# Kernel tuning notes

Hardware: AMD Instinct MI355X
Metric: run time of the kernel (lower is better)

Reference implementation:

```python
import jax, jax.numpy as jnp
import numpy as np

B, H, S, D = 2, 16, 1024, 64

def setup_inputs() -> dict:
    key = jax.random.key(0)
    k1, k2 = jax.random.split(key)
    # x1 is the output of a softmax (attention probabilities): non-negative, rows sum to 1
    logits = jax.random.normal(k1, (B, H, S, S), dtype=jnp.float32)
    x1 = jax.nn.softmax(logits, axis=-1)
    x2 = jax.random.normal(k2, (B, H, S, D), dtype=jnp.float32)
    return {"x1": x1, "x2": x2}

def reference(x1, x2):
    # Forward of EfficientMemoryGEMMWithSoftmax: exact batched GEMM.
    # (The outlier/low-bit compression only affects what is cached for backward;
    #  the forward output is the exact product.)
    return jnp.einsum('bhsk,bhkd->bhsd', x1, x2)
```

## Files before the change

### kernel.cpp

```cpp
#include <hip/hip_runtime.h>
#include <hip/hip_bf16.h>

typedef __attribute__((ext_vector_type(8))) short short8_t;
typedef __attribute__((ext_vector_type(4))) short short4_t;
typedef __attribute__((ext_vector_type(4))) float f32x4;

#define S_DIM   1024
#define D_DIM   64
#define BM      64
#define KC      64
#define NCHUNK  (S_DIM / KC)
#define BSTRIDE 72
#define THREADS 512

__device__ __forceinline__ ushort f2bf(float f) {
    __hip_bfloat16 h = __float2bfloat16(f);
    return __builtin_bit_cast(ushort, h);
}

#define SYNC() do { \
    __builtin_amdgcn_sched_barrier(0); \
    asm volatile("s_waitcnt lgkmcnt(0)"); \
    __builtin_amdgcn_s_barrier(); \
    __builtin_amdgcn_sched_barrier(0); \
} while (0)

__global__ __launch_bounds__(THREADS, 4)
void gemm_sm_kernel(const float* __restrict__ x1,
                    const float* __restrict__ x2,
                    float* __restrict__ out) {
    __shared__ ushort lds_a[2][BM * KC];
    __shared__ ushort lds_b[2][D_DIM * BSTRIDE];

    const int tid = threadIdx.x;
    const int bid = blockIdx.x;
    const int xcd = bid & 7;
    const int q   = bid >> 3;
    const int batch   = xcd * 4 + (q & 3);
    const int rowtile = q >> 2;
    const int row0    = rowtile * BM;

    const float* Abase = x1 + (size_t)batch * (S_DIM * S_DIM) + (size_t)row0 * S_DIM;
    const float* Bbase = x2 + (size_t)batch * (S_DIM * D_DIM);
    float*       Cbase = out + (size_t)batch * (S_DIM * D_DIM) + (size_t)row0 * D_DIM;

    const int w = tid >> 6;
    const int l = tid & 63;

    const int ar  = tid >> 3;
    const int ak8 = (tid & 7) * 8;
    const float* aptr = Abase + (size_t)ar * S_DIM + ak8;
    const int aw = (ar * KC + ak8) ^ ((ar & 7) << 3);

    const int bd  = l;
    const int bk0 = w * 4;

    const int wm = w >> 1, wn = w & 1;
    const int fr = l & 15, fg = l >> 4;
    int aidx[2], bidx[2][2];
    {
        const int row = wm * 16 + fr;
        #pragma unroll
        for (int ks = 0; ks < 2; ++ks)
            aidx[ks] = (row * KC + ks * 32 + fg * 8) ^ ((row & 7) << 3);
    }
    #pragma unroll
    for (int nf = 0; nf < 2; ++nf) {
        const int col = wn * 32 + nf * 16 + fr;
        #pragma unroll
        for (int ks = 0; ks < 2; ++ks)
            bidx[nf][ks] = col * BSTRIDE + ks * 32 + fg * 8;
    }

    float a0[8], a1[8], b0[8], b1[8];

    auto load_chunk = [&](int t, float (&A)[8], float (&B)[8]) {
        const float* p = aptr + t * KC;
        #pragma unroll
        for (int i = 0; i < 2; ++i) {
            float4 v = *reinterpret_cast<const float4*>(p + i * 4);
            A[i * 4 + 0] = v.x; A[i * 4 + 1] = v.y;
            A[i * 4 + 2] = v.z; A[i * 4 + 3] = v.w;
        }
        const float* bp = Bbase + (size_t)t * KC * D_DIM + bd;
        #pragma unroll
        for (int i = 0; i < 2; ++i)
            #pragma unroll
            for (int j = 0; j < 4; ++j)
                B[i * 4 + j] = bp[(bk0 + 32 * i + j) * D_DIM];
    };

    auto store_chunk = [&](ushort* la, ushort* lb,
                           const float (&A)[8], const float (&B)[8]) {
        short8_t v0;
        #pragma unroll
        for (int j = 0; j < 8; ++j) v0[j] = (short)f2bf(A[j]);
        *reinterpret_cast<short8_t*>(&la[aw]) = v0;
        #pragma unroll
        for (int i = 0; i < 2; ++i) {
            short4_t bv;
            #pragma unroll
            for (int j = 0; j < 4; ++j) bv[j] = (short)f2bf(B[i * 4 + j]);
            *reinterpret_cast<short4_t*>(&lb[bd * BSTRIDE + bk0 + 32 * i]) = bv;
        }
    };

    f32x4 acc[2];
    acc[0] = f32x4{0.f, 0.f, 0.f, 0.f};
    acc[1] = f32x4{0.f, 0.f, 0.f, 0.f};

    auto compute = [&](const ushort* la, const ushort* lb) {
        short8_t af[2], bf[2][2];
        #pragma unroll
        for (int ks = 0; ks < 2; ++ks)
            af[ks] = *reinterpret_cast<const short8_t*>(&la[aidx[ks]]);
        #pragma unroll
        for (int nf = 0; nf < 2; ++nf)
            #pragma unroll
            for (int ks = 0; ks < 2; ++ks)
                bf[nf][ks] = *reinterpret_cast<const short8_t*>(&lb[bidx[nf][ks]]);
        #pragma unroll
        for (int ks = 0; ks < 2; ++ks)
            #pragma unroll
            for (int nf = 0; nf < 2; ++nf)
                acc[nf] = __builtin_amdgcn_mfma_f32_16x16x32_bf16(
                    af[ks], bf[nf][ks], acc[nf], 0, 0, 0);
    };

    load_chunk(0, a0, b0);
    load_chunk(1, a1, b1);
    store_chunk(&lds_a[0][0], &lds_b[0][0], a0, b0);
    SYNC();

    #pragma unroll 1
    for (int ti = 0; ti < NCHUNK; ti += 2) {
        if (ti + 2 < NCHUNK) load_chunk(ti + 2, a0, b0);
        store_chunk(&lds_a[1][0], &lds_b[1][0], a1, b1);
        compute(&lds_a[0][0], &lds_b[0][0]);
        SYNC();

        if (ti + 3 < NCHUNK) load_chunk(ti + 3, a1, b1);
        if (ti + 2 < NCHUNK) store_chunk(&lds_a[0][0], &lds_b[0][0], a0, b0);
        compute(&lds_a[1][0], &lds_b[1][0]);
        SYNC();
    }

    #pragma unroll
    for (int nf = 0; nf < 2; ++nf)
        #pragma unroll
        for (int j = 0; j < 4; ++j) {
            const int r = wm * 16 + fg * 4 + j;
            const int c = wn * 32 + nf * 16 + fr;
            Cbase[(size_t)r * D_DIM + c] = acc[nf][j];
        }
}

extern "C" void kernel_launch(void* const* d_in, const int* in_sizes, int n_in,
                              void* d_out, int out_size, void* d_ws, size_t ws_size,
                              hipStream_t stream) {
    const float* x1 = (const float*)d_in[0];
    const float* x2 = (const float*)d_in[1];
    float* out = (float*)d_out;
    dim3 grid(512), block(THREADS);
    gemm_sm_kernel<<<grid, block, 0, stream>>>(x1, x2, out);
}
```

Baseline: 28.32 us.

## Load A fragments directly from global into registers, dropping the A LDS staging

```diff
diff --git a/kernel.cpp b/kernel.cpp
--- a/kernel.cpp
+++ b/kernel.cpp
@@ -29,7 +29,6 @@
 void gemm_sm_kernel(const float* __restrict__ x1,
                     const float* __restrict__ x2,
                     float* __restrict__ out) {
-    __shared__ ushort lds_a[2][BM * KC];
     __shared__ ushort lds_b[2][D_DIM * BSTRIDE];
 
     const int tid = threadIdx.x;
@@ -47,23 +46,15 @@
     const int w = tid >> 6;
     const int l = tid & 63;
 
-    const int ar  = tid >> 3;
-    const int ak8 = (tid & 7) * 8;
-    const float* aptr = Abase + (size_t)ar * S_DIM + ak8;
-    const int aw = (ar * KC + ak8) ^ ((ar & 7) << 3);
+    const int wm = w >> 1, wn = w & 1;
+    const int fr = l & 15, fg = l >> 4;
+
+    const float* arow = Abase + (size_t)(wm * 16 + fr) * S_DIM + fg * 8;
 
     const int bd  = l;
     const int bk0 = w * 4;
 
-    const int wm = w >> 1, wn = w & 1;
-    const int fr = l & 15, fg = l >> 4;
-    int aidx[2], bidx[2][2];
-    {
-        const int row = wm * 16 + fr;
-        #pragma unroll
-        for (int ks = 0; ks < 2; ++ks)
-            aidx[ks] = (row * KC + ks * 32 + fg * 8) ^ ((row & 7) << 3);
-    }
+    int bidx[2][2];
     #pragma unroll
     for (int nf = 0; nf < 2; ++nf) {
         const int col = wn * 32 + nf * 16 + fr;
@@ -72,16 +63,22 @@
             bidx[nf][ks] = col * BSTRIDE + ks * 32 + fg * 8;
     }
 
-    float a0[8], a1[8], b0[8], b1[8];
+    float araw0[16], araw1[16];
+    float breg0[8],  breg1[8];
 
-    auto load_chunk = [&](int t, float (&A)[8], float (&B)[8]) {
-        const float* p = aptr + t * KC;
+    auto loadA = [&](int t, float (&A)[16]) {
         #pragma unroll
-        for (int i = 0; i < 2; ++i) {
-            float4 v = *reinterpret_cast<const float4*>(p + i * 4);
-            A[i * 4 + 0] = v.x; A[i * 4 + 1] = v.y;
-            A[i * 4 + 2] = v.z; A[i * 4 + 3] = v.w;
+        for (int ks = 0; ks < 2; ++ks) {
+            const float* p = arow + t * KC + ks * 32;
+            float4 v0 = *reinterpret_cast<const float4*>(p);
+            float4 v1 = *reinterpret_cast<const float4*>(p + 4);
+            A[ks * 8 + 0] = v0.x; A[ks * 8 + 1] = v0.y;
+            A[ks * 8 + 2] = v0.z; A[ks * 8 + 3] = v0.w;
+            A[ks * 8 + 4] = v1.x; A[ks * 8 + 5] = v1.y;
+            A[ks * 8 + 6] = v1.z; A[ks * 8 + 7] = v1.w;
         }
+    };
+    auto loadB = [&](int t, float (&B)[8]) {
         const float* bp = Bbase + (size_t)t * KC * D_DIM + bd;
         #pragma unroll
         for (int i = 0; i < 2; ++i)
@@ -89,13 +86,7 @@
             for (int j = 0; j < 4; ++j)
                 B[i * 4 + j] = bp[(bk0 + 32 * i + j) * D_DIM];
     };
-
-    auto store_chunk = [&](ushort* la, ushort* lb,
-                           const float (&A)[8], const float (&B)[8]) {
-        short8_t v0;
-        #pragma unroll
-        for (int j = 0; j < 8; ++j) v0[j] = (short)f2bf(A[j]);
-        *reinterpret_cast<short8_t*>(&la[aw]) = v0;
+    auto storeB = [&](ushort* lb, const float (&B)[8]) {
         #pragma unroll
         for (int i = 0; i < 2; ++i) {
             short4_t bv;
@@ -109,11 +100,14 @@
     acc[0] = f32x4{0.f, 0.f, 0.f, 0.f};
     acc[1] = f32x4{0.f, 0.f, 0.f, 0.f};
 
-    auto compute = [&](const ushort* la, const ushort* lb) {
-        short8_t af[2], bf[2][2];
+    auto compute = [&](const float (&A)[16], const ushort* lb) {
+        short8_t af[2];
         #pragma unroll
         for (int ks = 0; ks < 2; ++ks)
-            af[ks] = *reinterpret_cast<const short8_t*>(&la[aidx[ks]]);
+            #pragma unroll
+            for (int j = 0; j < 8; ++j)
+                af[ks][j] = (short)f2bf(A[ks * 8 + j]);
+        short8_t bf[2][2];
         #pragma unroll
         for (int nf = 0; nf < 2; ++nf)
             #pragma unroll
@@ -127,21 +121,30 @@
                     af[ks], bf[nf][ks], acc[nf], 0, 0, 0);
     };
 
-    load_chunk(0, a0, b0);
-    load_chunk(1, a1, b1);
-    store_chunk(&lds_a[0][0], &lds_b[0][0], a0, b0);
+    loadA(0, araw0); loadB(0, breg0);
+    loadA(1, araw1); loadB(1, breg1);
+    storeB(&lds_b[0][0], breg0);
     SYNC();
 
     #pragma unroll 1
     for (int ti = 0; ti < NCHUNK; ti += 2) {
-        if (ti + 2 < NCHUNK) load_chunk(ti + 2, a0, b0);
-        store_chunk(&lds_a[1][0], &lds_b[1][0], a1, b1);
-        compute(&lds_a[0][0], &lds_b[0][0]);
+        {
+            float afrag[16];
+            #pragma unroll
+            for (int j = 0; j < 16; ++j) afrag[j] = araw0[j];
+            if (ti + 2 < NCHUNK) { loadA(ti + 2, araw0); loadB(ti + 2, breg0); }
+            storeB(&lds_b[1][0], breg1);
+            compute(afrag, &lds_b[0][0]);
+        }
         SYNC();
-
-        if (ti + 3 < NCHUNK) load_chunk(ti + 3, a1, b1);
-        if (ti + 2 < NCHUNK) store_chunk(&lds_a[0][0], &lds_b[0][0], a0, b0);
-        compute(&lds_a[1][0], &lds_b[1][0]);
+        {
+            float afrag[16];
+            #pragma unroll
+            for (int j = 0; j < 16; ++j) afrag[j] = araw1[j];
+            if (ti + 3 < NCHUNK) { loadA(ti + 3, araw1); loadB(ti + 3, breg1); }
+            if (ti + 2 < NCHUNK) storeB(&lds_b[0][0], breg0);
+            compute(afrag, &lds_b[1][0]);
+        }
         SYNC();
     }
 
```

After: 42.18 us. +48.9%, slower.
